# Kernel optimization log

Measured on AMD Instinct MI355X. Metric: run time of the kernel, lower is better.

The kernel has to match this reference:

```python
import jax, jax.numpy as jnp
import numpy as np

K = 7  # number of relaxed nearest neighbors (init arg k)
EXPM1_GUARD = 1e-7
LOG_HALF = float(np.log(0.5))

def log1mexp(x):
    # log(1 - exp(x)) for x <= 0, numerically stable (guard matches torch bw-path constant)
    t = x < LOG_HALF
    xa = jnp.where(t, x, -1.0)          # safe operand for log1p(-exp(.))
    xb = jnp.where(t, -1.0, x)          # safe operand for log(-expm1(.))
    ya = jnp.log1p(-jnp.exp(xa))
    yb = jnp.log(-jnp.expm1(xb) + EXPM1_GUARD)
    return jnp.where(t, ya, yb)

def setup_inputs() -> dict:
    key = jax.random.key(0)
    k1, k2, k3, k4 = jax.random.split(key, 4)
    b, n, m, o, e, f = 4, 8192, 2048, 64, 64, 128
    x = jax.random.normal(k1, (b, n, f), dtype=jnp.float32)
    xe = jax.random.normal(k2, (b, n, e), dtype=jnp.float32)
    ye = jax.random.normal(k3, (b, m, e), dtype=jnp.float32)
    log_temp_param = jnp.zeros((1,), dtype=jnp.float32)
    I = jax.random.randint(k4, (b, m, o), 0, n, dtype=jnp.int64)
    return {"x": x, "xe": xe, "ye": ye, "log_temp_param": log_temp_param, "I": I}

def reference(x, xe, ye, log_temp_param, I):
    b, n, f = x.shape
    m, o = I.shape[1], I.shape[2]
    bidx = jnp.arange(b)[:, None, None]          # [b,1,1] batch index for gathers

    # ---- compute_distances (indexed path): D[b,m,o] = -||xe[I] - ye||^2 ----
    xg_e = xe[bidx, I]                           # [b,m,o,e] gathered candidate embeddings
    diff = xg_e - ye[:, :, None, :]              # [b,m,o,e]
    D = -jnp.sum(diff * diff, axis=-1)           # [b,m,o]

    # ---- NeuralNearestNeighbors: temperature + k-step relaxed top-k ----
    temperature = jnp.exp(log_temp_param[0])     # log_temp_bias = log(1) = 0
    logits = (D / temperature).reshape(b * m, o)
    samples = []
    for _ in range(K):
        w = jax.nn.log_softmax(logits, axis=1)   # [b*m,o]
        samples.append(jnp.exp(w).reshape(b, m, o))
        logits = logits + log1mexp(w)
    W = jnp.stack(samples, axis=3)               # [b,m,o,K]

    # ---- aggregate_output: z[b,m,f,K] = sum_o W[b,m,o,K] * x[b, I[b,m,o], f] ----
    xg = x[bidx, I]                              # [b,m,o,f]
    z = jnp.einsum('bmok,bmof->bmfk', W, xg)     # [b,m,f,K]
    return z
```

## Files before the change

kernel.cpp:

```cpp
#include <hip/hip_runtime.h>
#include <math.h>

#define B_  4
#define N_  8192
#define M_  2048
#define O_  64
#define E_  64
#define F_  128
#define K_  7

__global__ __launch_bounds__(256, 6) void n3agg_kernel(
    const float* __restrict__ x, const float* __restrict__ xe,
    const float* __restrict__ ye, const float* __restrict__ log_temp,
    const int* __restrict__ I, float* __restrict__ out)
{
    __shared__ __align__(16) int   s_I[4][O_];
    __shared__ __align__(16) float s_ye[4][E_];
    __shared__ __align__(16) float s_W[4][K_][O_];

    const int tid  = threadIdx.x;
    const int w    = tid >> 6;
    const int lane = tid & 63;
    const int bid  = blockIdx.x * 4 + w;
    const int b    = bid >> 11;

    const int my_idx = I[(size_t)bid * O_ + lane];
    s_I[w][lane]  = my_idx;
    s_ye[w][lane] = ye[(size_t)bid * E_ + lane];

    const float4* xr4 = (const float4*)(xe + ((size_t)b * N_ + my_idx) * E_);
    const float4* ye4 = (const float4*)(&s_ye[w][0]);
    float S[16];
    #pragma unroll
    for (int q = 0; q < 4; ++q) {
        float4 xa = xr4[q],      ya = ye4[q];
        float4 xb = xr4[q + 4],  yb = ye4[q + 4];
        float4 xc = xr4[q + 8],  yc = ye4[q + 8];
        float4 xd = xr4[q + 12], yd = ye4[q + 12];
        float da, db, dc, dd;

        da = __fsub_rn(xa.x, ya.x); db = __fsub_rn(xb.x, yb.x);
        dc = __fsub_rn(xc.x, yc.x); dd = __fsub_rn(xd.x, yd.x);
        S[4*q+0] = __fadd_rn(__fadd_rn(__fmul_rn(da,da), __fmul_rn(db,db)),
                             __fadd_rn(__fmul_rn(dc,dc), __fmul_rn(dd,dd)));

        da = __fsub_rn(xa.y, ya.y); db = __fsub_rn(xb.y, yb.y);
        dc = __fsub_rn(xc.y, yc.y); dd = __fsub_rn(xd.y, yd.y);
        S[4*q+1] = __fadd_rn(__fadd_rn(__fmul_rn(da,da), __fmul_rn(db,db)),
                             __fadd_rn(__fmul_rn(dc,dc), __fmul_rn(dd,dd)));

        da = __fsub_rn(xa.z, ya.z); db = __fsub_rn(xb.z, yb.z);
        dc = __fsub_rn(xc.z, yc.z); dd = __fsub_rn(xd.z, yd.z);
        S[4*q+2] = __fadd_rn(__fadd_rn(__fmul_rn(da,da), __fmul_rn(db,db)),
                             __fadd_rn(__fmul_rn(dc,dc), __fmul_rn(dd,dd)));

        da = __fsub_rn(xa.w, ya.w); db = __fsub_rn(xb.w, yb.w);
        dc = __fsub_rn(xc.w, yc.w); dd = __fsub_rn(xd.w, yd.w);
        S[4*q+3] = __fadd_rn(__fadd_rn(__fmul_rn(da,da), __fmul_rn(db,db)),
                             __fadd_rn(__fmul_rn(dc,dc), __fmul_rn(dd,dd)));
    }
    float t8[8], t4[4], t2[2], res;
    #pragma unroll
    for (int l = 0; l < 8; ++l) t8[l] = __fadd_rn(S[l], S[l + 8]);
    #pragma unroll
    for (int l = 0; l < 4; ++l) t4[l] = __fadd_rn(t8[l], t8[l + 4]);
    t2[0] = __fadd_rn(t4[0], t4[2]);
    t2[1] = __fadd_rn(t4[1], t4[3]);
    res   = __fadd_rn(t2[0], t2[1]);

    const float temp = expf(log_temp[0]);
    float logit = __fdiv_rn(-res, temp);

    #pragma unroll
    for (int k = 0; k < K_; ++k) {
        float mx = logit;
        #pragma unroll
        for (int d = 1; d < 64; d <<= 1) mx = fmaxf(mx, __shfl_xor(mx, d));
        float sh = __fsub_rn(logit, mx);
        float ex = expf(sh);
        float t = __fadd_rn(ex, __shfl_xor(ex, 16));
        t = __fadd_rn(t, __shfl_xor(t, 32));
        t = __fadd_rn(t, __shfl_xor(t, 8));
        t = __fadd_rn(t, __shfl_xor(t, 4));
        t = __fadd_rn(t, __shfl_xor(t, 2));
        t = __fadd_rn(t, __shfl_xor(t, 1));
        const float sm = t;

        float wv = __fsub_rn(sh, logf(sm));
        s_W[w][k][lane] = expf(wv);

        float lm;
        if (wv < -0.69314718055994530942f) {
            lm = log1pf(-expf(wv));
        } else {
            lm = logf(__fadd_rn(-expm1f(wv), 1e-7f));
        }
        logit = __fadd_rn(logit, lm);
    }

    float acc0[K_], acc1[K_];
    #pragma unroll
    for (int k = 0; k < K_; ++k) { acc0[k] = 0.f; acc1[k] = 0.f; }
    const float* xbase = x + (size_t)b * N_ * F_ + 2 * lane;
    #pragma unroll 4
    for (int o = 0; o < O_; ++o) {
        const int idx = s_I[w][o];
        const float2 xv = *(const float2*)(xbase + (size_t)idx * F_);
        #pragma unroll
        for (int k = 0; k < K_; ++k) {
            const float wk = s_W[w][k][o];
            acc0[k] = fmaf(wk, xv.x, acc0[k]);
            acc1[k] = fmaf(wk, xv.y, acc1[k]);
        }
    }
    float* op = out + (size_t)bid * F_ * K_ + lane * 2 * K_;
    #pragma unroll
    for (int k = 0; k < K_; ++k) op[k] = acc0[k];
    #pragma unroll
    for (int k = 0; k < K_; ++k) op[K_ + k] = acc1[k];
}

extern "C" void kernel_launch(void* const* d_in, const int* in_sizes, int n_in,
                              void* d_out, int out_size, void* d_ws, size_t ws_size,
                              hipStream_t stream) {
    const float* x        = (const float*)d_in[0];
    const float* xe       = (const float*)d_in[1];
    const float* ye       = (const float*)d_in[2];
    const float* log_temp = (const float*)d_in[3];
    const int*   I        = (const int*)d_in[4];
    float* out = (float*)d_out;

    dim3 grid((B_ * M_) / 4);
    dim3 block(256);
    hipLaunchKernelGGL(n3agg_kernel, grid, block, 0, stream,
                       x, xe, ye, log_temp, I, out);
}
```

Before: 65.05 us.

## Restructure aggregation: float4 gathers, split neighbors across half-waves, vectorized stores

The aggregation loop now has each lane load a float4 of x features, with the two half-waves each handling alternate neighbors. Partial sums are combined with a cross-half shuffle. Softmax weights are kept in registers and written to shared memory transposed as [o][8], so each neighbor's seven weights load as two float4 reads instead of seven scalar reads. Outputs are written as contiguous float4 stores, and blocks shrink to two waves. This aims to cut shared-memory and global load instruction counts and to improve store coalescing, at the cost of more accumulator registers and an extra shuffle reduction.

```diff
diff --git a/kernel.cpp b/kernel.cpp
--- a/kernel.cpp
+++ b/kernel.cpp
@@ -9,19 +9,19 @@
 #define F_  128
 #define K_  7
 
-__global__ __launch_bounds__(256, 6) void n3agg_kernel(
+__global__ __launch_bounds__(128, 6) void n3agg_kernel(
     const float* __restrict__ x, const float* __restrict__ xe,
     const float* __restrict__ ye, const float* __restrict__ log_temp,
     const int* __restrict__ I, float* __restrict__ out)
 {
-    __shared__ __align__(16) int   s_I[4][O_];
-    __shared__ __align__(16) float s_ye[4][E_];
-    __shared__ __align__(16) float s_W[4][K_][O_];
+    __shared__ __align__(16) int   s_I[2][O_];
+    __shared__ __align__(16) float s_ye[2][E_];
+    __shared__ __align__(16) float s_W[2][O_][8];
 
     const int tid  = threadIdx.x;
     const int w    = tid >> 6;
     const int lane = tid & 63;
-    const int bid  = blockIdx.x * 4 + w;
+    const int bid  = blockIdx.x * 2 + w;
     const int b    = bid >> 11;
 
     const int my_idx = I[(size_t)bid * O_ + lane];
@@ -71,6 +71,7 @@
     const float temp = expf(log_temp[0]);
     float logit = __fdiv_rn(-res, temp);
 
+    float wreg[K_];
     #pragma unroll
     for (int k = 0; k < K_; ++k) {
         float mx = logit;
@@ -87,7 +88,7 @@
         const float sm = t;
 
         float wv = __fsub_rn(sh, logf(sm));
-        s_W[w][k][lane] = expf(wv);
+        wreg[k] = expf(wv);
 
         float lm;
         if (wv < -0.69314718055994530942f) {
@@ -97,27 +98,52 @@
         }
         logit = __fadd_rn(logit, lm);
     }
+    {
+        float* wp = &s_W[w][lane][0];
+        *(float4*)wp       = make_float4(wreg[0], wreg[1], wreg[2], wreg[3]);
+        *(float2*)(wp + 4) = make_float2(wreg[4], wreg[5]);
+        wp[6] = wreg[6];
+    }
 
-    float acc0[K_], acc1[K_];
+    const int h  = lane >> 5;
+    const int fl = lane & 31;
+    float acc[4][K_];
     #pragma unroll
-    for (int k = 0; k < K_; ++k) { acc0[k] = 0.f; acc1[k] = 0.f; }
-    const float* xbase = x + (size_t)b * N_ * F_ + 2 * lane;
-    #pragma unroll 4
-    for (int o = 0; o < O_; ++o) {
+    for (int q = 0; q < 4; ++q)
+        #pragma unroll
+        for (int k = 0; k < K_; ++k) acc[q][k] = 0.f;
+
+    const float* xb = x + (size_t)b * N_ * F_ + 4 * fl;
+    #pragma unroll 2
+    for (int t = 0; t < 32; ++t) {
+        const int o = 2 * t + h;
         const int idx = s_I[w][o];
-        const float2 xv = *(const float2*)(xbase + (size_t)idx * F_);
+        const float4 xv = *(const float4*)(xb + (size_t)idx * F_);
+        const float* wrow = &s_W[w][o][0];
+        const float4 wa = *(const float4*)(wrow);
+        const float4 wb = *(const float4*)(wrow + 4);
+        const float wk[K_] = {wa.x, wa.y, wa.z, wa.w, wb.x, wb.y, wb.z};
         #pragma unroll
         for (int k = 0; k < K_; ++k) {
-            const float wk = s_W[w][k][o];
-            acc0[k] = fmaf(wk, xv.x, acc0[k]);
-            acc1[k] = fmaf(wk, xv.y, acc1[k]);
+            acc[0][k] = fmaf(wk[k], xv.x, acc[0][k]);
+            acc[1][k] = fmaf(wk[k], xv.y, acc[1][k]);
+            acc[2][k] = fmaf(wk[k], xv.z, acc[2][k]);
+            acc[3][k] = fmaf(wk[k], xv.w, acc[3][k]);
         }
     }
-    float* op = out + (size_t)bid * F_ * K_ + lane * 2 * K_;
     #pragma unroll
-    for (int k = 0; k < K_; ++k) op[k] = acc0[k];
-    #pragma unroll
-    for (int k = 0; k < K_; ++k) op[K_ + k] = acc1[k];
+    for (int q = 0; q < 4; ++q)
+        #pragma unroll
+        for (int k = 0; k < K_; ++k)
+            acc[q][k] += __shfl_xor(acc[q][k], 32);
+
+    if (lane < 32) {
+        const float* af = &acc[0][0];
+        float4* op4 = (float4*)(out + (size_t)bid * F_ * K_ + fl * 28);
+        #pragma unroll
+        for (int j = 0; j < 7; ++j)
+            op4[j] = make_float4(af[4*j], af[4*j+1], af[4*j+2], af[4*j+3]);
+    }
 }
 
 extern "C" void kernel_launch(void* const* d_in, const int* in_sizes, int n_in,
@@ -130,8 +156,8 @@
     const int*   I        = (const int*)d_in[4];
     float* out = (float*)d_out;
 
-    dim3 grid((B_ * M_) / 4);
-    dim3 block(256);
+    dim3 grid((B_ * M_) / 2);
+    dim3 block(128);
     hipLaunchKernelGGL(n3agg_kernel, grid, block, 0, stream,
                        x, xe, ye, log_temp, I, out);
 }
```

Measured after the change: 64.60 us. About the same (-0.7%).
